# Performance work log

Measured on AMD Instinct MI355X. Metric: run time of the kernel, lower is better.

The kernel has to match this reference:

```python
import jax, jax.numpy as jnp
import numpy as np
import math

D_MODEL = 1024
NUM_HEADS = 16
D_K = D_MODEL // NUM_HEADS
SEQ = 2048
BATCH = 2


def setup_inputs() -> dict:
    key = jax.random.key(0)
    ks = jax.random.split(key, 11)
    s = 1.0 / math.sqrt(D_MODEL)
    return {
        "query": jax.random.normal(ks[0], (SEQ, BATCH, D_MODEL), jnp.float32),
        "key": jax.random.normal(ks[1], (SEQ, BATCH, D_MODEL), jnp.float32),
        "value": jax.random.normal(ks[2], (SEQ, BATCH, D_MODEL), jnp.float32),
        "Wq": jax.random.normal(ks[3], (D_MODEL, D_MODEL), jnp.float32) * s,
        "bq": jnp.zeros((D_MODEL,), jnp.float32),
        "Wk": jax.random.normal(ks[4], (D_MODEL, D_MODEL), jnp.float32) * s,
        "bk": jnp.zeros((D_MODEL,), jnp.float32),
        "Wv": jax.random.normal(ks[5], (D_MODEL, D_MODEL), jnp.float32) * s,
        "bv": jnp.zeros((D_MODEL,), jnp.float32),
        "Wo": jax.random.normal(ks[6], (D_MODEL, D_MODEL), jnp.float32) * s,
        "bo": jnp.zeros((D_MODEL,), jnp.float32),
    }


def _split_heads(x):
    # [S, B, D] -> [S, B, H, d_k]
    S, B, _ = x.shape
    return x.reshape(S, B, NUM_HEADS, D_K)


def reference(query, key, value, Wq, bq, Wk, bk, Wv, bv, Wo, bo):
    # torch Linear: y = x @ W.T + b
    q = _split_heads(query @ Wq.T + bq)   # [S,B,H,dk]
    k = _split_heads(key @ Wk.T + bk)
    v = _split_heads(value @ Wv.T + bv)
    # score[q,k,b,h] = sum_d q[q,b,h,d] k[k,b,h,d]
    score = jnp.einsum('qbhd,kbhd->qkbh', q, k) / math.sqrt(D_K)
    attn = jax.nn.softmax(score, axis=1)  # Softmax(dim=1) == over key axis
    out = jnp.einsum('qkbh,kbhd->qbhd', attn, v)  # [S,B,H,dk]
    S, B = out.shape[0], out.shape[1]
    out = out.reshape(S, B, NUM_HEADS * D_K)
    return out @ Wo.T + bo
```

## Files before the change

kernel.cpp:

```cpp
#include <hip/hip_runtime.h>

typedef unsigned short u16;
typedef short s16x8 __attribute__((ext_vector_type(8)));
typedef short s16x4 __attribute__((ext_vector_type(4)));
typedef float f32x4 __attribute__((ext_vector_type(4)));

#define MFMA_BF16(A,B,C) __builtin_amdgcn_mfma_f32_16x16x32_bf16(A,B,C,0,0,0)

#if defined(__has_builtin)
#if __has_builtin(__builtin_amdgcn_mfma_f32_16x16x16bf16_1k)
#define HAVE_MFMA16 1
#define MFMA16(A,B,C) __builtin_amdgcn_mfma_f32_16x16x16bf16_1k(A,B,C,0,0,0)
#endif
#endif

static constexpr int DMODEL = 1024;
static constexpr int SEQn   = 2048;
static constexpr int BATCH  = 2;
static constexpr int NH     = 16;
static constexpr int DKn    = 64;
static constexpr int ROWST  = BATCH*DMODEL;
static constexpr float QSCALE = 0.18033688011112042f;

__device__ __forceinline__ u16 f2bf(float f) {
    unsigned u = __builtin_bit_cast(unsigned, f);
    u += 0x7FFFu + ((u >> 16) & 1u);
    return (u16)(u >> 16);
}

#if defined(__has_builtin)
#if __has_builtin(__builtin_amdgcn_cvt_pk_bf16_f32)
#define HAVE_PKBF16 1
#endif
#endif
#ifdef HAVE_PKBF16
typedef __bf16 bf16x2 __attribute__((ext_vector_type(2)));
__device__ __forceinline__ unsigned pk2bf(float a, float b) {
    bf16x2 t = __builtin_amdgcn_cvt_pk_bf16_f32(a, b);
    return __builtin_bit_cast(unsigned, t);
}
#else
__device__ __forceinline__ unsigned pk2bf(float a, float b) {
    return (unsigned)f2bf(a) | ((unsigned)f2bf(b) << 16);
}
#endif

__device__ __forceinline__ void gld_lds16(const u16* g, u16* l) {
    __builtin_amdgcn_global_load_lds(
        (const __attribute__((address_space(1))) void*)g,
        (__attribute__((address_space(3))) void*)l,
        16, 0, 0);
}

__global__ void cvt_bf16(const float* __restrict__ q, const float* __restrict__ k,
                         const float* __restrict__ v, const float* __restrict__ wq,
                         const float* __restrict__ wk, const float* __restrict__ wv,
                         const float* __restrict__ wo,
                         u16* __restrict__ qb, u16* __restrict__ kb, u16* __restrict__ vb,
                         u16* __restrict__ wqb, u16* __restrict__ wkb, u16* __restrict__ wvb,
                         u16* __restrict__ wob)
{
    const int z = blockIdx.z;
    const float* S; u16* D; size_t n;
    switch (z) {
        case 0: S = q;  D = qb;  n = 4194304; break;
        case 1: S = k;  D = kb;  n = 4194304; break;
        case 2: S = v;  D = vb;  n = 4194304; break;
        case 3: S = wq; D = wqb; n = 1048576; break;
        case 4: S = wk; D = wkb; n = 1048576; break;
        case 5: S = wv; D = wvb; n = 1048576; break;
        default: S = wo; D = wob; n = 1048576; break;
    }
    const size_t i = ((size_t)blockIdx.x * 256 + threadIdx.x) * 8;
    if (i >= n) return;
    float4 a = *(const float4*)(S + i);
    float4 b = *(const float4*)(S + i + 4);
    uint4 pk;
    pk.x = pk2bf(a.x, a.y); pk.y = pk2bf(a.z, a.w);
    pk.z = pk2bf(b.x, b.y); pk.w = pk2bf(b.z, b.w);
    *(uint4*)(D + i) = pk;
}

template<bool FINAL>
__global__ __launch_bounds__(256, 2)
void gemm_bt(const u16* __restrict__ A0, const u16* __restrict__ A1, const u16* __restrict__ A2,
             const u16* __restrict__ W0, const u16* __restrict__ W1, const u16* __restrict__ W2,
             const float* __restrict__ B0, const float* __restrict__ B1, const float* __restrict__ B2,
             void* __restrict__ O0, void* __restrict__ O1, void* __restrict__ O2)
{
    const u16* A; const u16* W; const float* bias; void* Outv;
    const int z = blockIdx.z;
    if (z == 0)      { A = A0; W = W0; bias = B0; Outv = O0; }
    else if (z == 1) { A = A1; W = W1; bias = B1; Outv = O1; }
    else             { A = A2; W = W2; bias = B2; Outv = O2; }

    __shared__ alignas(16) u16 SH[FINAL ? 128*128 : 129*128];
    u16* As = SH;
    u16* Bs = SH + 128*64;

    const int tid  = threadIdx.x;
    const int wave = tid >> 6, lane = tid & 63;
    const int quad = lane >> 4, col = lane & 15;
    const int wm = wave & 1, wn = wave >> 1;
    const int m0 = blockIdx.y * 128, n0 = blockIdx.x * 128;

    f32x4 acc[4][4];
#pragma unroll
    for (int i = 0; i < 4; ++i)
#pragma unroll
        for (int j = 0; j < 4; ++j) acc[i][j] = f32x4{0.f,0.f,0.f,0.f};

    for (int kt = 0; kt < DMODEL/64; ++kt) {
        if (kt) __syncthreads();
        const int k0 = kt*64;
#pragma unroll
        for (int i = 0; i < 4; ++i) {
            const int chunk = (i*4 + wave)*64 + lane;
            const int row = chunk >> 3;
            const int kk = ((chunk & 7) ^ (row & 7)) * 8;
            gld_lds16(A + (size_t)(m0 + row)*DMODEL + (k0 + kk), &As[(i*4 + wave)*512]);
            gld_lds16(W + (size_t)(n0 + row)*DMODEL + (k0 + kk), &Bs[(i*4 + wave)*512]);
        }
        __syncthreads();
#pragma unroll
        for (int ks = 0; ks < 2; ++ks) {
            s16x8 af[4], bfr[4];
#pragma unroll
            for (int t = 0; t < 4; ++t) {
                const int ra = wm*64 + t*16 + col;
                af[t]  = *(const s16x8*)&As[ra*64 + (((ks*4 + quad) ^ (ra & 7))*8)];
                const int rb = wn*64 + t*16 + col;
                bfr[t] = *(const s16x8*)&Bs[rb*64 + (((ks*4 + quad) ^ (rb & 7))*8)];
            }
#pragma unroll
            for (int i = 0; i < 4; ++i)
#pragma unroll
                for (int j = 0; j < 4; ++j)
                    acc[i][j] = MFMA_BF16(af[i], bfr[j], acc[i][j]);
        }
    }

    float bv[4];
#pragma unroll
    for (int j = 0; j < 4; ++j) bv[j] = bias[n0 + wn*64 + j*16 + col];

    if (FINAL) {
#pragma unroll
        for (int i = 0; i < 4; ++i)
#pragma unroll
            for (int j = 0; j < 4; ++j) {
                const int n = n0 + wn*64 + j*16 + col;
#pragma unroll
                for (int r = 0; r < 4; ++r) {
                    const int m = m0 + wm*64 + i*16 + quad*4 + r;
                    ((float*)Outv)[(size_t)m*DMODEL + n] = acc[i][j][r] + bv[j];
                }
            }
    } else {
        const float osc = (z == 0) ? QSCALE : 1.f;
        const int SST = (z == 2) ? 129 : 128;
        __syncthreads();
#pragma unroll
        for (int i = 0; i < 4; ++i)
#pragma unroll
            for (int j = 0; j < 4; ++j) {
                const int nl = wn*64 + j*16 + col;
#pragma unroll
                for (int r = 0; r < 4; ++r) {
                    const int ml = wm*64 + i*16 + quad*4 + r;
                    SH[ml*SST + nl] = f2bf((acc[i][j][r] + bv[j])*osc);
                }
            }
        __syncthreads();
        u16* Out = (u16*)Outv;
        if (z < 2) {
#pragma unroll
            for (int t = 0; t < 8; ++t) {
                const int c = t*256 + tid;
                const int ml = c >> 4, n8 = (c & 15)*8;
                uint4 x = *(const uint4*)&SH[ml*128 + n8];
                *(uint4*)(Out + (size_t)(m0 + ml)*DMODEL + n0 + n8) = x;
            }
        } else {
            const int s0 = m0 >> 1;
#pragma unroll
            for (int t = 0; t < 8; ++t) {
                const int c = t*256 + tid;
                const int sc = c & 7;
                const int nl = (c >> 3) & 127;
                const int bb = c >> 10;
                u16 e[8];
#pragma unroll
                for (int j = 0; j < 8; ++j)
                    e[j] = SH[((sc*8 + j)*2 + bb)*129 + nl];
                uint4 x; __builtin_memcpy(&x, e, 16);
                const int ng = n0 + nl, hh = ng >> 6, dd = ng & 63;
                *(uint4*)(Out + (((size_t)bb*NH + hh)*DKn + dd)*SEQn + s0 + sc*8) = x;
            }
        }
    }
}

__global__ __launch_bounds__(256, 4)
void attn_fwd(const u16* __restrict__ Q, const u16* __restrict__ K,
              const u16* __restrict__ Vt, u16* __restrict__ O)
{
    __shared__ alignas(16) u16 Ks[128*64];
    __shared__ alignas(16) u16 Vs[64*128];

    const int qt = blockIdx.x, bh = blockIdx.y;
    const int b = bh >> 4, h = bh & 15;
    const int tid = threadIdx.x;
    const int wave = tid >> 6, lane = tid & 63;
    const int quad = lane >> 4, col = lane & 15;

    const u16* Qh = Q + b*DMODEL + h*DKn;
    const u16* Kh = K + b*DMODEL + h*DKn;
    const u16* Vh = Vt + (size_t)bh*DKn*SEQn;

    const int q0 = qt*64 + wave*16;
    s16x8 qf[2];
#pragma unroll
    for (int ks = 0; ks < 2; ++ks)
        qf[ks] = *(const s16x8*)(Qh + (size_t)(q0 + col)*ROWST + ks*32 + quad*8);

    const short ONEBF = (short)0x3F80;
    const s16x4 ones = {ONEBF, ONEBF, ONEBF, ONEBF};

    f32x4 o[4];
    f32x4 lacc = f32x4{0.f,0.f,0.f,0.f};
#pragma unroll
    for (int dt = 0; dt < 4; ++dt) o[dt] = f32x4{0.f,0.f,0.f,0.f};

    for (int kt = 0; kt < SEQn/128; ++kt) {
        __syncthreads();
#pragma unroll
        for (int i = 0; i < 4; ++i) {
            {
                const int chunk = (i*4 + wave)*64 + lane;
                const int row = chunk >> 3;
                const int kk = ((chunk & 7) ^ (row & 7))*8;
                gld_lds16(Kh + (size_t)(kt*128 + row)*ROWST + kk, &Ks[(i*4 + wave)*512]);
            }
            {
                const int chunk = (i*4 + wave)*64 + lane;
                const int d = chunk >> 4;
                const int kk = ((chunk & 15) ^ (d & 15))*8;
                gld_lds16(Vh + (size_t)d*SEQn + kt*128 + kk, &Vs[(i*4 + wave)*512]);
            }
        }
        __syncthreads();

        f32x4 sfr[8];
#pragma unroll
        for (int nt = 0; nt < 8; ++nt) sfr[nt] = f32x4{0.f,0.f,0.f,0.f};
#pragma unroll
        for (int ks = 0; ks < 2; ++ks) {
            s16x8 kf[8];
#pragma unroll
            for (int nt = 0; nt < 8; ++nt) {
                const int key = nt*16 + col;
                kf[nt] = *(const s16x8*)&Ks[key*64 + (((ks*4 + quad) ^ (key & 7))*8)];
            }
#pragma unroll
            for (int nt = 0; nt < 8; ++nt)
                sfr[nt] = MFMA_BF16(kf[nt], qf[ks], sfr[nt]);
        }

        s16x4 pk[8];
#pragma unroll
        for (int nt = 0; nt < 8; ++nt) {
            float p0 = __builtin_amdgcn_exp2f(sfr[nt][0]);
            float p1 = __builtin_amdgcn_exp2f(sfr[nt][1]);
            float p2 = __builtin_amdgcn_exp2f(sfr[nt][2]);
            float p3 = __builtin_amdgcn_exp2f(sfr[nt][3]);
            unsigned w[2] = { pk2bf(p0, p1), pk2bf(p2, p3) };
            __builtin_memcpy(&pk[nt], w, 8);
        }

#ifdef HAVE_MFMA16
#pragma unroll
        for (int c = 0; c < 8; ++c) {
            lacc = MFMA16(ones, pk[c], lacc);
#pragma unroll
            for (int dt = 0; dt < 4; ++dt) {
                const int d = dt*16 + col;
                const s16x4 vfr = *(const s16x4*)&Vs[d*128 + (((c*2 + (quad>>1)) ^ (d & 15))*8) + (quad & 1)*4];
                o[dt] = MFMA16(vfr, pk[c], o[dt]);
            }
        }
#else
        const int a0 = (32*(quad & 1) + col)*4;
        const s16x8 ones8 = {ONEBF,ONEBF,ONEBF,ONEBF,ONEBF,ONEBF,ONEBF,ONEBF};
#pragma unroll
        for (int ksp = 0; ksp < 4; ++ksp) {
            int pA[2], pB[2];
            __builtin_memcpy(pA, &pk[ksp*2], 8);
            __builtin_memcpy(pB, &pk[ksp*2 + 1], 8);
            int w[4];
#pragma unroll
            for (int hh = 0; hh < 2; ++hh) {
                const int ad = a0 + hh*64;
                const int xA0 = __builtin_amdgcn_ds_bpermute(ad, pA[0]);
                const int xA1 = __builtin_amdgcn_ds_bpermute(ad, pA[1]);
                const int xB0 = __builtin_amdgcn_ds_bpermute(ad, pB[0]);
                const int xB1 = __builtin_amdgcn_ds_bpermute(ad, pB[1]);
                w[hh*2]     = (quad >= 2) ? xB0 : xA0;
                w[hh*2 + 1] = (quad >= 2) ? xB1 : xA1;
            }
            s16x8 pfr; __builtin_memcpy(&pfr, w, 16);
            lacc = MFMA_BF16(ones8, pfr, lacc);
#pragma unroll
            for (int dt = 0; dt < 4; ++dt) {
                const int d = dt*16 + col;
                const s16x8 vfr = *(const s16x8*)&Vs[d*128 + (((ksp*4 + quad) ^ (d & 15))*8)];
                o[dt] = MFMA_BF16(vfr, pfr, o[dt]);
            }
        }
#endif
    }

    const float inv = 1.f / lacc[0];
    const int srow = q0 + col;
#pragma unroll
    for (int dt = 0; dt < 4; ++dt) {
        uint2 pko;
        pko.x = pk2bf(o[dt][0]*inv, o[dt][1]*inv);
        pko.y = pk2bf(o[dt][2]*inv, o[dt][3]*inv);
        *(uint2*)(O + ((size_t)srow*BATCH + b)*DMODEL + h*DKn + dt*16 + quad*4) = pko;
    }
}

extern "C" void kernel_launch(void* const* d_in, const int* in_sizes, int n_in,
                              void* d_out, int out_size, void* d_ws, size_t ws_size,
                              hipStream_t stream)
{
    const float* q  = (const float*)d_in[0];
    const float* k  = (const float*)d_in[1];
    const float* v  = (const float*)d_in[2];
    const float* Wq = (const float*)d_in[3];
    const float* bq = (const float*)d_in[4];
    const float* Wk = (const float*)d_in[5];
    const float* bk = (const float*)d_in[6];
    const float* Wv = (const float*)d_in[7];
    const float* bv = (const float*)d_in[8];
    const float* Wo = (const float*)d_in[9];
    const float* bo = (const float*)d_in[10];
    float* out = (float*)d_out;

    const size_t N = (size_t)SEQn * BATCH * DMODEL;
    const size_t NW = (size_t)DMODEL * DMODEL;
    u16* qb  = (u16*)d_ws;
    u16* kb  = qb + N;
    u16* vb  = kb + N;
    u16* wqb = vb + N;
    u16* wkb = wqb + NW;
    u16* wvb = wkb + NW;
    u16* wob = wvb + NW;
    u16* Qw  = wob + NW;
    u16* Kw  = Qw + N;
    u16* Vtw = Kw + N;
    u16* AO  = qb;

    cvt_bf16<<<dim3(2048, 1, 7), 256, 0, stream>>>(q, k, v, Wq, Wk, Wv, Wo,
                                                   qb, kb, vb, wqb, wkb, wvb, wob);
    gemm_bt<false><<<dim3(8, 32, 3), 256, 0, stream>>>(qb, kb, vb, wqb, wkb, wvb,
                                                       bq, bk, bv, Qw, Kw, Vtw);
    attn_fwd<<<dim3(32, 32), 256, 0, stream>>>(Qw, Kw, Vtw, AO);
    gemm_bt<true><<<dim3(8, 32, 1), 256, 0, stream>>>(AO, AO, AO, wob, wob, wob,
                                                      bo, bo, bo, out, out, out);
}
```

Baseline: 230.8 us.

## Process two query groups per wave in attention and sum denominators in registers

Each wave now handles 32 query rows instead of 16. Every K and V fragment read from LDS is reused by two MFMAs, and the K/V tile loads are amortized over 128 queries per block, so the grid is halved. The softmax denominator is no longer computed with a ones-vector MFMA. Each lane accumulates its exp sum in fp32 and the partial sums are combined with cross-lane shuffles at the end. This adds register pressure (launch bounds lowered to 2 blocks) and gives fewer blocks, which may reduce occupancy and latency hiding.

Measured after the change: 234.6 us. Within noise of the previous version (+1.6%).

```diff
diff --git a/kernel.cpp b/kernel.cpp
--- a/kernel.cpp
+++ b/kernel.cpp
@@ -201,7 +201,7 @@
     }
 }
 
-__global__ __launch_bounds__(256, 4)
+__global__ __launch_bounds__(256, 2)
 void attn_fwd(const u16* __restrict__ Q, const u16* __restrict__ K,
               const u16* __restrict__ Vt, u16* __restrict__ O)
 {
@@ -218,19 +218,20 @@
     const u16* Kh = K + b*DMODEL + h*DKn;
     const u16* Vh = Vt + (size_t)bh*DKn*SEQn;
 
-    const int q0 = qt*64 + wave*16;
-    s16x8 qf[2];
-#pragma unroll
-    for (int ks = 0; ks < 2; ++ks)
-        qf[ks] = *(const s16x8*)(Qh + (size_t)(q0 + col)*ROWST + ks*32 + quad*8);
-
-    const short ONEBF = (short)0x3F80;
-    const s16x4 ones = {ONEBF, ONEBF, ONEBF, ONEBF};
-
-    f32x4 o[4];
-    f32x4 lacc = f32x4{0.f,0.f,0.f,0.f};
-#pragma unroll
-    for (int dt = 0; dt < 4; ++dt) o[dt] = f32x4{0.f,0.f,0.f,0.f};
+    const int q0 = qt*128 + wave*32;
+    s16x8 qf[2][2];
+#pragma unroll
+    for (int qg = 0; qg < 2; ++qg)
+#pragma unroll
+        for (int ks = 0; ks < 2; ++ks)
+            qf[qg][ks] = *(const s16x8*)(Qh + (size_t)(q0 + qg*16 + col)*ROWST + ks*32 + quad*8);
+
+    f32x4 o[2][4];
+    float dsum[2] = {0.f, 0.f};
+#pragma unroll
+    for (int qg = 0; qg < 2; ++qg)
+#pragma unroll
+        for (int dt = 0; dt < 4; ++dt) o[qg][dt] = f32x4{0.f,0.f,0.f,0.f};
 
     for (int kt = 0; kt < SEQn/128; ++kt) {
         __syncthreads();
@@ -251,83 +252,98 @@
         }
         __syncthreads();
 
-        f32x4 sfr[8];
-#pragma unroll
-        for (int nt = 0; nt < 8; ++nt) sfr[nt] = f32x4{0.f,0.f,0.f,0.f};
+        f32x4 sfr[2][8];
+#pragma unroll
+        for (int qg = 0; qg < 2; ++qg)
+#pragma unroll
+            for (int nt = 0; nt < 8; ++nt) sfr[qg][nt] = f32x4{0.f,0.f,0.f,0.f};
 #pragma unroll
         for (int ks = 0; ks < 2; ++ks) {
-            s16x8 kf[8];
 #pragma unroll
             for (int nt = 0; nt < 8; ++nt) {
                 const int key = nt*16 + col;
-                kf[nt] = *(const s16x8*)&Ks[key*64 + (((ks*4 + quad) ^ (key & 7))*8)];
-            }
-#pragma unroll
-            for (int nt = 0; nt < 8; ++nt)
-                sfr[nt] = MFMA_BF16(kf[nt], qf[ks], sfr[nt]);
-        }
-
-        s16x4 pk[8];
-#pragma unroll
-        for (int nt = 0; nt < 8; ++nt) {
-            float p0 = __builtin_amdgcn_exp2f(sfr[nt][0]);
-            float p1 = __builtin_amdgcn_exp2f(sfr[nt][1]);
-            float p2 = __builtin_amdgcn_exp2f(sfr[nt][2]);
-            float p3 = __builtin_amdgcn_exp2f(sfr[nt][3]);
-            unsigned w[2] = { pk2bf(p0, p1), pk2bf(p2, p3) };
-            __builtin_memcpy(&pk[nt], w, 8);
-        }
+                const s16x8 kf = *(const s16x8*)&Ks[key*64 + (((ks*4 + quad) ^ (key & 7))*8)];
+                sfr[0][nt] = MFMA_BF16(kf, qf[0][ks], sfr[0][nt]);
+                sfr[1][nt] = MFMA_BF16(kf, qf[1][ks], sfr[1][nt]);
+            }
+        }
+
+        s16x4 pk[2][8];
+#pragma unroll
+        for (int qg = 0; qg < 2; ++qg)
+#pragma unroll
+            for (int nt = 0; nt < 8; ++nt) {
+                float p0 = __builtin_amdgcn_exp2f(sfr[qg][nt][0]);
+                float p1 = __builtin_amdgcn_exp2f(sfr[qg][nt][1]);
+                float p2 = __builtin_amdgcn_exp2f(sfr[qg][nt][2]);
+                float p3 = __builtin_amdgcn_exp2f(sfr[qg][nt][3]);
+                dsum[qg] += (p0 + p1) + (p2 + p3);
+                unsigned w[2] = { pk2bf(p0, p1), pk2bf(p2, p3) };
+                __builtin_memcpy(&pk[qg][nt], w, 8);
+            }
 
 #ifdef HAVE_MFMA16
 #pragma unroll
         for (int c = 0; c < 8; ++c) {
-            lacc = MFMA16(ones, pk[c], lacc);
 #pragma unroll
             for (int dt = 0; dt < 4; ++dt) {
                 const int d = dt*16 + col;
                 const s16x4 vfr = *(const s16x4*)&Vs[d*128 + (((c*2 + (quad>>1)) ^ (d & 15))*8) + (quad & 1)*4];
-                o[dt] = MFMA16(vfr, pk[c], o[dt]);
+                o[0][dt] = MFMA16(vfr, pk[0][c], o[0][dt]);
+                o[1][dt] = MFMA16(vfr, pk[1][c], o[1][dt]);
             }
         }
 #else
         const int a0 = (32*(quad & 1) + col)*4;
-        const s16x8 ones8 = {ONEBF,ONEBF,ONEBF,ONEBF,ONEBF,ONEBF,ONEBF,ONEBF};
-#pragma unroll
-        for (int ksp = 0; ksp < 4; ++ksp) {
-            int pA[2], pB[2];
-            __builtin_memcpy(pA, &pk[ksp*2], 8);
-            __builtin_memcpy(pB, &pk[ksp*2 + 1], 8);
-            int w[4];
-#pragma unroll
-            for (int hh = 0; hh < 2; ++hh) {
-                const int ad = a0 + hh*64;
-                const int xA0 = __builtin_amdgcn_ds_bpermute(ad, pA[0]);
-                const int xA1 = __builtin_amdgcn_ds_bpermute(ad, pA[1]);
-                const int xB0 = __builtin_amdgcn_ds_bpermute(ad, pB[0]);
-                const int xB1 = __builtin_amdgcn_ds_bpermute(ad, pB[1]);
-                w[hh*2]     = (quad >= 2) ? xB0 : xA0;
-                w[hh*2 + 1] = (quad >= 2) ? xB1 : xA1;
-            }
-            s16x8 pfr; __builtin_memcpy(&pfr, w, 16);
-            lacc = MFMA_BF16(ones8, pfr, lacc);
-#pragma unroll
-            for (int dt = 0; dt < 4; ++dt) {
-                const int d = dt*16 + col;
-                const s16x8 vfr = *(const s16x8*)&Vs[d*128 + (((ksp*4 + quad) ^ (d & 15))*8)];
-                o[dt] = MFMA_BF16(vfr, pfr, o[dt]);
-            }
-        }
-#endif
-    }
-
-    const float inv = 1.f / lacc[0];
-    const int srow = q0 + col;
-#pragma unroll
-    for (int dt = 0; dt < 4; ++dt) {
-        uint2 pko;
-        pko.x = pk2bf(o[dt][0]*inv, o[dt][1]*inv);
-        pko.y = pk2bf(o[dt][2]*inv, o[dt][3]*inv);
-        *(uint2*)(O + ((size_t)srow*BATCH + b)*DMODEL + h*DKn + dt*16 + quad*4) = pko;
+#pragma unroll
+        for (int qg = 0; qg < 2; ++qg) {
+#pragma unroll
+            for (int ksp = 0; ksp < 4; ++ksp) {
+                int pA[2], pB[2];
+                __builtin_memcpy(pA, &pk[qg][ksp*2], 8);
+                __builtin_memcpy(pB, &pk[qg][ksp*2 + 1], 8);
+                int w[4];
+#pragma unroll
+                for (int hh = 0; hh < 2; ++hh) {
+                    const int ad = a0 + hh*64;
+                    const int xA0 = __builtin_amdgcn_ds_bpermute(ad, pA[0]);
+                    const int xA1 = __builtin_amdgcn_ds_bpermute(ad, pA[1]);
+                    const int xB0 = __builtin_amdgcn_ds_bpermute(ad, pB[0]);
+                    const int xB1 = __builtin_amdgcn_ds_bpermute(ad, pB[1]);
+                    w[hh*2]     = (quad >= 2) ? xB0 : xA0;
+                    w[hh*2 + 1] = (quad >= 2) ? xB1 : xA1;
+                }
+                s16x8 pfr; __builtin_memcpy(&pfr, w, 16);
+#pragma unroll
+                for (int dt = 0; dt < 4; ++dt) {
+                    const int d = dt*16 + col;
+                    const s16x8 vfr = *(const s16x8*)&Vs[d*128 + (((ksp*4 + quad) ^ (d & 15))*8)];
+                    o[qg][dt] = MFMA_BF16(vfr, pfr, o[qg][dt]);
+                }
+            }
+        }
+#endif
+    }
+
+    float inv[2];
+#pragma unroll
+    for (int qg = 0; qg < 2; ++qg) {
+        float d = dsum[qg];
+        d += __shfl_xor(d, 16, 64);
+        d += __shfl_xor(d, 32, 64);
+        inv[qg] = 1.f / d;
+    }
+
+#pragma unroll
+    for (int qg = 0; qg < 2; ++qg) {
+        const int srow = q0 + qg*16 + col;
+#pragma unroll
+        for (int dt = 0; dt < 4; ++dt) {
+            uint2 pko;
+            pko.x = pk2bf(o[qg][dt][0]*inv[qg], o[qg][dt][1]*inv[qg]);
+            pko.y = pk2bf(o[qg][dt][2]*inv[qg], o[qg][dt][3]*inv[qg]);
+            *(uint2*)(O + ((size_t)srow*BATCH + b)*DMODEL + h*DKn + dt*16 + quad*4) = pko;
+        }
     }
 }
 
@@ -366,7 +382,7 @@
                                                    qb, kb, vb, wqb, wkb, wvb, wob);
     gemm_bt<false><<<dim3(8, 32, 3), 256, 0, stream>>>(qb, kb, vb, wqb, wkb, wvb,
                                                        bq, bk, bv, Qw, Kw, Vtw);
-    attn_fwd<<<dim3(32, 32), 256, 0, stream>>>(Qw, Kw, Vtw, AO);
+    attn_fwd<<<dim3(16, 32), 256, 0, stream>>>(Qw, Kw, Vtw, AO);
     gemm_bt<true><<<dim3(8, 32, 1), 256, 0, stream>>>(AO, AO, AO, wob, wob, wob,
                                                       bo, bo, bo, out, out, out);
 }
```

## Add 256x256-tile QKV projection GEMM with 4-stage async LDS pipeline

Applied to the files above, without the earlier changes.

Replaces the 128x128 QKV projection GEMM with a new kernel that uses 512-thread blocks computing 256x256 output tiles. It streams K in 32-wide slices through a 4-slot LDS ring via direct global-to-LDS loads, with explicit vmcnt waits and XOR swizzling. The aim is more operand reuse per loaded byte and overlap of loads with MFMA work. The cost is higher register pressure (128 accumulators per thread), 128KB of LDS, and only 192 blocks, which may leave some CUs underused.

After: 229.5 us. About the same (-0.5%).

```diff
diff --git a/kernel.cpp b/kernel.cpp
--- a/kernel.cpp
+++ b/kernel.cpp
@@ -81,6 +81,157 @@
     *(uint4*)(D + i) = pk;
 }
 
+__global__ __launch_bounds__(512, 2)
+void gemm_qkv(const u16* __restrict__ A0, const u16* __restrict__ A1, const u16* __restrict__ A2,
+              const u16* __restrict__ W0, const u16* __restrict__ W1, const u16* __restrict__ W2,
+              const float* __restrict__ B0, const float* __restrict__ B1, const float* __restrict__ B2,
+              void* __restrict__ O0, void* __restrict__ O1, void* __restrict__ O2)
+{
+    const u16* A; const u16* W; const float* bias; void* Outv;
+    const int z = blockIdx.z;
+    if (z == 0)      { A = A0; W = W0; bias = B0; Outv = O0; }
+    else if (z == 1) { A = A1; W = W1; bias = B1; Outv = O1; }
+    else             { A = A2; W = W2; bias = B2; Outv = O2; }
+
+    __shared__ alignas(16) u16 SH[65536];
+
+    const int tid  = threadIdx.x;
+    const int wave = tid >> 6, lane = tid & 63;
+    const int quad = lane >> 4, col = lane & 15;
+    const int wr = wave >> 2;
+    const int wn = wave & 3;
+    const int m0 = blockIdx.y * 256, n0 = blockIdx.x * 256;
+
+    f32x4 acc[8][4];
+#pragma unroll
+    for (int i = 0; i < 8; ++i)
+#pragma unroll
+        for (int j = 0; j < 4; ++j) acc[i][j] = f32x4{0.f,0.f,0.f,0.f};
+
+    auto stageT = [&](int t) {
+        const int slot = t & 3;
+        const int k0 = t * 32;
+        u16* Ad = SH + slot * 8192;
+        u16* Bd = SH + 32768 + slot * 8192;
+#pragma unroll
+        for (int i = 0; i < 2; ++i) {
+            const int idx = i*512 + wave*64 + lane;
+            const int row = idx >> 2;
+            const int s = idx & 3;
+            const int g = s ^ ((row >> 1) & 3);
+            gld_lds16(A + (size_t)(m0 + row)*DMODEL + k0 + g*8, Ad + (i*512 + wave*64)*8);
+            gld_lds16(W + (size_t)(n0 + row)*DMODEL + k0 + g*8, Bd + (i*512 + wave*64)*8);
+        }
+    };
+
+    auto compute = [&](int slot) {
+        const u16* As_ = SH + slot * 8192;
+        const u16* Bs_ = SH + 32768 + slot * 8192;
+        s16x8 bfr[4], af[4];
+#pragma unroll
+        for (int fj = 0; fj < 4; ++fj) {
+            const int rb = wn*64 + fj*16 + col;
+            bfr[fj] = *(const s16x8*)&Bs_[rb*32 + (quad ^ ((rb >> 1) & 3))*8];
+        }
+#pragma unroll
+        for (int fi = 0; fi < 4; ++fi) {
+            const int ra = wr*128 + fi*16 + col;
+            af[fi] = *(const s16x8*)&As_[ra*32 + (quad ^ ((ra >> 1) & 3))*8];
+        }
+        __builtin_amdgcn_s_setprio(1);
+#pragma unroll
+        for (int fi = 0; fi < 4; ++fi)
+#pragma unroll
+            for (int fj = 0; fj < 4; ++fj)
+                acc[fi][fj] = MFMA_BF16(af[fi], bfr[fj], acc[fi][fj]);
+        __builtin_amdgcn_s_setprio(0);
+#pragma unroll
+        for (int fi = 0; fi < 4; ++fi) {
+            const int ra = wr*128 + (4 + fi)*16 + col;
+            af[fi] = *(const s16x8*)&As_[ra*32 + (quad ^ ((ra >> 1) & 3))*8];
+        }
+        __builtin_amdgcn_s_setprio(1);
+#pragma unroll
+        for (int fi = 0; fi < 4; ++fi)
+#pragma unroll
+            for (int fj = 0; fj < 4; ++fj)
+                acc[4 + fi][fj] = MFMA_BF16(af[fi], bfr[fj], acc[4 + fi][fj]);
+        __builtin_amdgcn_s_setprio(0);
+    };
+
+    stageT(0); stageT(1); stageT(2);
+
+    for (int t = 0; t < 30; ++t) {
+        asm volatile("s_waitcnt vmcnt(8)" ::: "memory");
+        __builtin_amdgcn_s_barrier();
+        asm volatile("" ::: "memory");
+        if (t < 29) stageT(t + 3);
+        compute(t & 3);
+    }
+    asm volatile("s_waitcnt vmcnt(4)" ::: "memory");
+    __builtin_amdgcn_s_barrier();
+    asm volatile("" ::: "memory");
+    compute(2);
+    asm volatile("s_waitcnt vmcnt(0)" ::: "memory");
+    __builtin_amdgcn_s_barrier();
+    asm volatile("" ::: "memory");
+    compute(3);
+
+    float bv[4];
+#pragma unroll
+    for (int fj = 0; fj < 4; ++fj) bv[fj] = bias[n0 + wn*64 + fj*16 + col];
+
+    if (z < 2) {
+        u16* Out = (u16*)Outv;
+        const float osc = (z == 0) ? QSCALE : 1.f;
+#pragma unroll
+        for (int fi = 0; fi < 8; ++fi)
+#pragma unroll
+            for (int fj = 0; fj < 4; ++fj) {
+                const int n = n0 + wn*64 + fj*16 + col;
+#pragma unroll
+                for (int r = 0; r < 4; ++r) {
+                    const int m = m0 + wr*128 + fi*16 + quad*4 + r;
+                    Out[(size_t)m*DMODEL + n] = f2bf((acc[fi][fj][r] + bv[fj])*osc);
+                }
+            }
+    } else {
+        u16* Out = (u16*)Outv;
+        u16* T = SH;
+#pragma unroll
+        for (int p = 0; p < 2; ++p) {
+            __syncthreads();
+            if (wr == p) {
+#pragma unroll
+                for (int fi = 0; fi < 8; ++fi)
+#pragma unroll
+                    for (int fj = 0; fj < 4; ++fj) {
+                        const int nl = wn*64 + fj*16 + col;
+#pragma unroll
+                        for (int r = 0; r < 4; ++r)
+                            T[(fi*16 + quad*4 + r)*257 + nl] = f2bf(acc[fi][fj][r] + bv[fj]);
+                    }
+            }
+            __syncthreads();
+            const int s0 = (m0 >> 1) + p*64;
+#pragma unroll
+            for (int t = 0; t < 8; ++t) {
+                const int c = t*512 + tid;
+                const int sc = c & 7;
+                const int nl = (c >> 3) & 255;
+                const int bb = c >> 11;
+                u16 e[8];
+#pragma unroll
+                for (int j = 0; j < 8; ++j)
+                    e[j] = T[((sc*8 + j)*2 + bb)*257 + nl];
+                uint4 x; __builtin_memcpy(&x, e, 16);
+                const int ng = n0 + nl, hh = ng >> 6, dd = ng & 63;
+                *(uint4*)(Out + (((size_t)bb*NH + hh)*DKn + dd)*SEQn + s0 + sc*8) = x;
+            }
+        }
+    }
+}
+
 template<bool FINAL>
 __global__ __launch_bounds__(256, 2)
 void gemm_bt(const u16* __restrict__ A0, const u16* __restrict__ A1, const u16* __restrict__ A2,
@@ -364,8 +515,8 @@
 
     cvt_bf16<<<dim3(2048, 1, 7), 256, 0, stream>>>(q, k, v, Wq, Wk, Wv, Wo,
                                                    qb, kb, vb, wqb, wkb, wvb, wob);
-    gemm_bt<false><<<dim3(8, 32, 3), 256, 0, stream>>>(qb, kb, vb, wqb, wkb, wvb,
-                                                       bq, bk, bv, Qw, Kw, Vtw);
+    gemm_qkv<<<dim3(4, 16, 3), 512, 0, stream>>>(qb, kb, vb, wqb, wkb, wvb,
+                                                 bq, bk, bv, Qw, Kw, Vtw);
     attn_fwd<<<dim3(32, 32), 256, 0, stream>>>(Qw, Kw, Vtw, AO);
     gemm_bt<true><<<dim3(8, 32, 1), 256, 0, stream>>>(AO, AO, AO, wob, wob, wob,
                                                       bo, bo, bo, out, out, out);
```

## Triple-buffer GEMM K-tiles with async LDS loads overlapping MFMA compute

Applied to the files above, without the earlier changes.

Rewrites the projection GEMM main loop as a 3-slot ring buffer of 32-wide K tiles. Global-to-LDS loads for tile t+2 are issued before computing tile t, with a single barrier per iteration and explicit vmcnt waits. This hides load latency that the old load-sync-compute-sync loop exposed. It also raises the launch-bound occupancy to 3 blocks, uses a new XOR swizzle for the narrower tile, and bumps wave priority around the MFMA burst. The cost is larger shared memory per block and more barriers per unit of work, since the K steps are halved in size.

After: 224.2 us. 2.9% less time.

```diff
diff --git a/kernel.cpp b/kernel.cpp
--- a/kernel.cpp
+++ b/kernel.cpp
@@ -82,11 +82,11 @@
 }
 
 template<bool FINAL>
-__global__ __launch_bounds__(256, 2)
-void gemm_bt(const u16* __restrict__ A0, const u16* __restrict__ A1, const u16* __restrict__ A2,
-             const u16* __restrict__ W0, const u16* __restrict__ W1, const u16* __restrict__ W2,
-             const float* __restrict__ B0, const float* __restrict__ B1, const float* __restrict__ B2,
-             void* __restrict__ O0, void* __restrict__ O1, void* __restrict__ O2)
+__global__ __launch_bounds__(256, 3)
+void gemm_p(const u16* __restrict__ A0, const u16* __restrict__ A1, const u16* __restrict__ A2,
+            const u16* __restrict__ W0, const u16* __restrict__ W1, const u16* __restrict__ W2,
+            const float* __restrict__ B0, const float* __restrict__ B1, const float* __restrict__ B2,
+            void* __restrict__ O0, void* __restrict__ O1, void* __restrict__ O2)
 {
     const u16* A; const u16* W; const float* bias; void* Outv;
     const int z = blockIdx.z;
@@ -94,9 +94,7 @@
     else if (z == 1) { A = A1; W = W1; bias = B1; Outv = O1; }
     else             { A = A2; W = W2; bias = B2; Outv = O2; }
 
-    __shared__ alignas(16) u16 SH[FINAL ? 128*128 : 129*128];
-    u16* As = SH;
-    u16* Bs = SH + 128*64;
+    __shared__ alignas(16) u16 SH[24576];
 
     const int tid  = threadIdx.x;
     const int wave = tid >> 6, lane = tid & 63;
@@ -110,35 +108,54 @@
 #pragma unroll
         for (int j = 0; j < 4; ++j) acc[i][j] = f32x4{0.f,0.f,0.f,0.f};
 
-    for (int kt = 0; kt < DMODEL/64; ++kt) {
-        if (kt) __syncthreads();
-        const int k0 = kt*64;
-#pragma unroll
-        for (int i = 0; i < 4; ++i) {
-            const int chunk = (i*4 + wave)*64 + lane;
-            const int row = chunk >> 3;
-            const int kk = ((chunk & 7) ^ (row & 7)) * 8;
-            gld_lds16(A + (size_t)(m0 + row)*DMODEL + (k0 + kk), &As[(i*4 + wave)*512]);
-            gld_lds16(W + (size_t)(n0 + row)*DMODEL + (k0 + kk), &Bs[(i*4 + wave)*512]);
-        }
-        __syncthreads();
-#pragma unroll
-        for (int ks = 0; ks < 2; ++ks) {
-            s16x8 af[4], bfr[4];
-#pragma unroll
-            for (int t = 0; t < 4; ++t) {
-                const int ra = wm*64 + t*16 + col;
-                af[t]  = *(const s16x8*)&As[ra*64 + (((ks*4 + quad) ^ (ra & 7))*8)];
-                const int rb = wn*64 + t*16 + col;
-                bfr[t] = *(const s16x8*)&Bs[rb*64 + (((ks*4 + quad) ^ (rb & 7))*8)];
-            }
-#pragma unroll
-            for (int i = 0; i < 4; ++i)
-#pragma unroll
-                for (int j = 0; j < 4; ++j)
-                    acc[i][j] = MFMA_BF16(af[i], bfr[j], acc[i][j]);
-        }
-    }
+    auto stageT = [&](int t) {
+        const int slot = t % 3;
+        const int k0 = t * 32;
+        u16* Ad = SH + slot*4096;
+        u16* Bd = SH + 12288 + slot*4096;
+#pragma unroll
+        for (int i = 0; i < 2; ++i) {
+            const int idx = i*256 + wave*64 + lane;
+            const int row = idx >> 2;
+            const int g = (idx & 3) ^ ((row >> 1) & 3);
+            gld_lds16(A + (size_t)(m0 + row)*DMODEL + k0 + g*8, Ad + (i*256 + wave*64)*8);
+            gld_lds16(W + (size_t)(n0 + row)*DMODEL + k0 + g*8, Bd + (i*256 + wave*64)*8);
+        }
+    };
+
+    auto compute = [&](int slot) {
+        const u16* As_ = SH + slot*4096;
+        const u16* Bs_ = SH + 12288 + slot*4096;
+        s16x8 af[4], bfr[4];
+#pragma unroll
+        for (int t4 = 0; t4 < 4; ++t4) {
+            const int ra = wm*64 + t4*16 + col;
+            af[t4]  = *(const s16x8*)&As_[ra*32 + ((quad ^ ((ra >> 1) & 3))*8)];
+            const int rb = wn*64 + t4*16 + col;
+            bfr[t4] = *(const s16x8*)&Bs_[rb*32 + ((quad ^ ((rb >> 1) & 3))*8)];
+        }
+        __builtin_amdgcn_s_setprio(1);
+#pragma unroll
+        for (int i = 0; i < 4; ++i)
+#pragma unroll
+            for (int j = 0; j < 4; ++j)
+                acc[i][j] = MFMA_BF16(af[i], bfr[j], acc[i][j]);
+        __builtin_amdgcn_s_setprio(0);
+    };
+
+    stageT(0); stageT(1);
+
+    for (int t = 0; t < 31; ++t) {
+        asm volatile("s_waitcnt vmcnt(4)" ::: "memory");
+        __builtin_amdgcn_s_barrier();
+        asm volatile("" ::: "memory");
+        if (t < 30) stageT(t + 2);
+        compute(t % 3);
+    }
+    asm volatile("s_waitcnt vmcnt(0)" ::: "memory");
+    __builtin_amdgcn_s_barrier();
+    asm volatile("" ::: "memory");
+    compute(31 % 3);
 
     float bv[4];
 #pragma unroll
@@ -364,9 +381,9 @@
 
     cvt_bf16<<<dim3(2048, 1, 7), 256, 0, stream>>>(q, k, v, Wq, Wk, Wv, Wo,
                                                    qb, kb, vb, wqb, wkb, wvb, wob);
-    gemm_bt<false><<<dim3(8, 32, 3), 256, 0, stream>>>(qb, kb, vb, wqb, wkb, wvb,
-                                                       bq, bk, bv, Qw, Kw, Vtw);
+    gemm_p<false><<<dim3(8, 32, 3), 256, 0, stream>>>(qb, kb, vb, wqb, wkb, wvb,
+                                                      bq, bk, bv, Qw, Kw, Vtw);
     attn_fwd<<<dim3(32, 32), 256, 0, stream>>>(Qw, Kw, Vtw, AO);
-    gemm_bt<true><<<dim3(8, 32, 1), 256, 0, stream>>>(AO, AO, AO, wob, wob, wob,
-                                                      bo, bo, bo, out, out, out);
-}
+    gemm_p<true><<<dim3(8, 32, 1), 256, 0, stream>>>(AO, AO, AO, wob, wob, wob,
+                                                     bo, bo, bo, out, out, out);
+}
```
